# Kernel tuning notes

Measured on AMD Instinct MI355X. Metric: run time of the kernel, lower is better.

The kernel has to match this reference:

```python
import jax, jax.numpy as jnp
import numpy as np

_EPS = 1e-10
_SHIFT = 1


def setup_inputs() -> dict:
    key = jax.random.key(0)
    k1, k2 = jax.random.split(key)
    n_rays, n_samples = 262144, 128
    alpha = jax.random.uniform(k1, (n_rays, n_samples), dtype=jnp.float32)
    rgbs = jax.random.uniform(k2, (n_rays, n_samples, 3), dtype=jnp.float32)
    return {"alpha": alpha, "rgbs": rgbs}


def reference(alpha, rgbs):
    # transmittance: cumulative product of (1 - alpha + eps) along samples
    trans = jnp.cumprod(1.0 - alpha + _EPS, axis=-1)
    # shift right by _SHIFT and fill the first _SHIFT entries with 1
    # (equivalent to torch.roll + trans[..., :shift] = 1 for shift <= n_samples)
    ones = jnp.ones(alpha.shape[:-1] + (_SHIFT,), dtype=alpha.dtype)
    trans = jnp.concatenate([ones, trans[..., :-_SHIFT]], axis=-1)
    weights = trans * alpha  # [n_rays, n_samples]
    # weighted sum over samples -> rendered rgb [n_rays, 3]
    rgbs_rendered = jnp.einsum("rs,rsc->rc", weights, rgbs)
    return rgbs_rendered
```

## Files before the change

### kernel.cpp

```cpp
#include <hip/hip_runtime.h>

#define N_SAMPLES 128
#define EPS 1e-10f

__global__ __launch_bounds__(256) void VolumeRenderer_14336600834233_kernel(
    const float* __restrict__ alpha,
    const float* __restrict__ rgbs,
    float* __restrict__ out,
    int n_rays)
{
    const int wavesPerBlock = blockDim.x >> 6;
    const int ray  = blockIdx.x * wavesPerBlock + (threadIdx.x >> 6);
    const int lane = threadIdx.x & 63;
    if (ray >= n_rays) return;

    const float2* a2 = (const float2*)alpha;
    const float2 a = a2[(size_t)ray * (N_SAMPLES / 2) + lane];
    const float f0 = 1.0f - a.x + EPS;
    const float f1 = 1.0f - a.y + EPS;
    const float p  = f0 * f1;

    float incl = p;
    #pragma unroll
    for (int off = 1; off < 64; off <<= 1) {
        float v = __shfl_up(incl, off, 64);
        if (lane >= off) incl *= v;
    }
    float excl = __shfl_up(incl, 1, 64);
    if (lane == 0) excl = 1.0f;

    const float w0 = a.x * excl;
    const float w1 = a.y * excl * f0;

    const float2* rg = (const float2*)rgbs;
    const size_t base = (size_t)ray * (N_SAMPLES * 3 / 2) + 3 * lane;
    const float2 v0 = rg[base + 0];
    const float2 v1 = rg[base + 1];
    const float2 v2 = rg[base + 2];

    float cr = fmaf(w0, v0.x, w1 * v1.y);
    float cg = fmaf(w0, v0.y, w1 * v2.x);
    float cb = fmaf(w0, v1.x, w1 * v2.y);

    #pragma unroll
    for (int off = 32; off; off >>= 1) {
        cr += __shfl_xor(cr, off, 64);
        cg += __shfl_xor(cg, off, 64);
        cb += __shfl_xor(cb, off, 64);
    }

    if (lane == 0) {
        float* o = out + (size_t)ray * 3;
        o[0] = cr;
        o[1] = cg;
        o[2] = cb;
    }
}

extern "C" void kernel_launch(void* const* d_in, const int* in_sizes, int n_in,
                              void* d_out, int out_size, void* d_ws, size_t ws_size,
                              hipStream_t stream) {
    const float* alpha = (const float*)d_in[0];
    const float* rgbs  = (const float*)d_in[1];
    float* out = (float*)d_out;

    const int n_rays = in_sizes[0] / N_SAMPLES;

    const int block = 256;
    const int waves_per_block = block / 64;
    const int grid = (n_rays + waves_per_block - 1) / waves_per_block;

    VolumeRenderer_14336600834233_kernel<<<grid, block, 0, stream>>>(
        alpha, rgbs, out, n_rays);
}
```

Measured before the change: 94.00 us.

## Process two rays per wave with float4 loads and nontemporal memory ops

Each wave now handles two rays with 32 lanes each. Every lane loads four alpha values and three float4 rgb vectors, replacing the earlier float2 loads, so the scan and the reduction each need one fewer shuffle step. Loads and stores use nontemporal hints to avoid polluting the cache on this streaming, bandwidth-bound kernel. Each lane does more register work in the serial per-lane product chain, and the grid is halved.

```diff
diff --git a/kernel.cpp b/kernel.cpp
--- a/kernel.cpp
+++ b/kernel.cpp
@@ -3,73 +3,82 @@
 #define N_SAMPLES 128
 #define EPS 1e-10f
 
+typedef float f4 __attribute__((ext_vector_type(4)));
+
 __global__ __launch_bounds__(256) void VolumeRenderer_14336600834233_kernel(
-    const float* __restrict__ alpha,
-    const float* __restrict__ rgbs,
+    const f4* __restrict__ alpha4,
+    const f4* __restrict__ rgb4,
     float* __restrict__ out,
     int n_rays)
 {
     const int wavesPerBlock = blockDim.x >> 6;
-    const int ray  = blockIdx.x * wavesPerBlock + (threadIdx.x >> 6);
+    const int wave = blockIdx.x * wavesPerBlock + (threadIdx.x >> 6);
     const int lane = threadIdx.x & 63;
+    const int g    = lane >> 5;
+    const int l    = lane & 31;
+    const int ray  = wave * 2 + g;
     if (ray >= n_rays) return;
 
-    const float2* a2 = (const float2*)alpha;
-    const float2 a = a2[(size_t)ray * (N_SAMPLES / 2) + lane];
-    const float f0 = 1.0f - a.x + EPS;
-    const float f1 = 1.0f - a.y + EPS;
-    const float p  = f0 * f1;
+    const f4 av = __builtin_nontemporal_load(&alpha4[(size_t)ray * 32 + l]);
+    const float f0 = 1.0f - av.x + EPS;
+    const float f1 = 1.0f - av.y + EPS;
+    const float f2 = 1.0f - av.z + EPS;
+    const float f3 = 1.0f - av.w + EPS;
+    const float p  = (f0 * f1) * (f2 * f3);
 
     float incl = p;
     #pragma unroll
-    for (int off = 1; off < 64; off <<= 1) {
+    for (int off = 1; off < 32; off <<= 1) {
         float v = __shfl_up(incl, off, 64);
-        if (lane >= off) incl *= v;
+        incl = (l >= off) ? incl * v : incl;
     }
     float excl = __shfl_up(incl, 1, 64);
-    if (lane == 0) excl = 1.0f;
+    if (l == 0) excl = 1.0f;
 
-    const float w0 = a.x * excl;
-    const float w1 = a.y * excl * f0;
+    const float w0 = av.x * excl;
+    const float t1 = excl * f0;
+    const float w1 = av.y * t1;
+    const float t2 = t1 * f1;
+    const float w2 = av.z * t2;
+    const float w3 = av.w * (t2 * f2);
 
-    const float2* rg = (const float2*)rgbs;
-    const size_t base = (size_t)ray * (N_SAMPLES * 3 / 2) + 3 * lane;
-    const float2 v0 = rg[base + 0];
-    const float2 v1 = rg[base + 1];
-    const float2 v2 = rg[base + 2];
+    const size_t rb = (size_t)ray * 96 + (size_t)l * 3;
+    const f4 x0 = __builtin_nontemporal_load(&rgb4[rb + 0]);
+    const f4 x1 = __builtin_nontemporal_load(&rgb4[rb + 1]);
+    const f4 x2 = __builtin_nontemporal_load(&rgb4[rb + 2]);
 
-    float cr = fmaf(w0, v0.x, w1 * v1.y);
-    float cg = fmaf(w0, v0.y, w1 * v2.x);
-    float cb = fmaf(w0, v1.x, w1 * v2.y);
+    float cr = fmaf(w0, x0.x, fmaf(w1, x0.w, fmaf(w2, x1.z, w3 * x2.y)));
+    float cg = fmaf(w0, x0.y, fmaf(w1, x1.x, fmaf(w2, x1.w, w3 * x2.z)));
+    float cb = fmaf(w0, x0.z, fmaf(w1, x1.y, fmaf(w2, x2.x, w3 * x2.w)));
 
     #pragma unroll
-    for (int off = 32; off; off >>= 1) {
+    for (int off = 16; off; off >>= 1) {
         cr += __shfl_xor(cr, off, 64);
         cg += __shfl_xor(cg, off, 64);
         cb += __shfl_xor(cb, off, 64);
     }
 
-    if (lane == 0) {
+    if (l == 0) {
         float* o = out + (size_t)ray * 3;
-        o[0] = cr;
-        o[1] = cg;
-        o[2] = cb;
+        __builtin_nontemporal_store(cr, o + 0);
+        __builtin_nontemporal_store(cg, o + 1);
+        __builtin_nontemporal_store(cb, o + 2);
     }
 }
 
 extern "C" void kernel_launch(void* const* d_in, const int* in_sizes, int n_in,
                               void* d_out, int out_size, void* d_ws, size_t ws_size,
                               hipStream_t stream) {
-    const float* alpha = (const float*)d_in[0];
-    const float* rgbs  = (const float*)d_in[1];
+    const f4* alpha4 = (const f4*)d_in[0];
+    const f4* rgb4   = (const f4*)d_in[1];
     float* out = (float*)d_out;
 
     const int n_rays = in_sizes[0] / N_SAMPLES;
 
     const int block = 256;
-    const int waves_per_block = block / 64;
-    const int grid = (n_rays + waves_per_block - 1) / waves_per_block;
+    const int rays_per_block = (block / 64) * 2;
+    const int grid = (n_rays + rays_per_block - 1) / rays_per_block;
 
     VolumeRenderer_14336600834233_kernel<<<grid, block, 0, stream>>>(
-        alpha, rgbs, out, n_rays);
+        alpha4, rgb4, out, n_rays);
 }
```

Result: slower. 116.2 us (+23.6%).
